# Kernel optimization log

Hardware: AMD Instinct MI355X
Metric: run time of the kernel (lower is better)

## Reference

```python
import jax, jax.numpy as jnp
import numpy as np
from itertools import combinations

# Module config: I=16, J=8 -> n_qubits = I + I + J = 40, k = 2
N_QUBITS = 40
K = 2
GATES = [(i, i + 1) for i in range(N_QUBITS - 1)]  # 39 RBS gates (ladder)
BATCH = 64


def _build_rbs_matrices():
    """Replicates RBS_Unitaries: for each gate (a,b) over the Hamming-weight-K
    basis of N_QUBITS qubits, build (A, B, C) with U(theta) = cos(theta)*A + sin(theta)*B + C.
    A: identity on states where exactly one of (a,b) is occupied (cos part).
    B: antisymmetric coupling swapping occupation of a<->b (sin part).
    C: identity on states where a,b have equal occupation (untouched part).
    """
    basis = list(combinations(range(N_QUBITS), K))
    idx = {s: i for i, s in enumerate(basis)}
    D = len(basis)  # binom(40, 2) = 780
    G = len(GATES)
    A = np.zeros((G, D, D), np.float32)
    B = np.zeros((G, D, D), np.float32)
    C = np.zeros((G, D, D), np.float32)
    for g, (a, b) in enumerate(GATES):
        for s in basis:
            i = idx[s]
            in_a, in_b = (a in s), (b in s)
            if in_a != in_b:
                A[g, i, i] = 1.0
                if in_a:  # pair |..1_a..0_b..> with |..0_a..1_b..>
                    t = tuple(sorted((set(s) - {a}) | {b}))
                    j = idx[t]
                    B[g, j, i] = 1.0
                    B[g, i, j] = -1.0
            else:
                C[g, i, i] = 1.0
    return A, B, C


def setup_inputs() -> dict:
    key = jax.random.key(0)
    k1, k2 = jax.random.split(key)
    A, B, C = _build_rbs_matrices()
    D = A.shape[-1]
    input_state = jax.random.normal(k1, (BATCH, D, D), dtype=jnp.float32)
    angles = jax.random.uniform(k2, (len(GATES),), dtype=jnp.float32)  # torch.rand(()) per gate
    return {
        "input_state": input_state,
        "angles": angles,
        "A": jnp.asarray(A),
        "B": jnp.asarray(B),
        "C": jnp.asarray(C),
    }


def reference(input_state, angles, A, B, C):
    """Sequentially applies each RBS gate: rho <- U rho U^T (real matrices)."""
    rho0 = input_state.astype(jnp.float32)

    def step(rho, gate):
        Ag, Bg, Cg, th = gate
        U = jnp.cos(th) * Ag + jnp.sin(th) * Bg + Cg  # [D, D]
        rho = jnp.einsum('ij,bjk->bik', U, rho)        # U @ rho
        rho = jnp.einsum('bik,lk->bil', rho, U)        # (U rho) @ U^T
        return rho, None

    out, _ = jax.lax.scan(step, rho0, (A, B, C, angles))
    return out
```

## Files before the change

### kernel.cpp

```cpp
#include <hip/hip_runtime.h>

#define D   780
#define NG  39
#define NP  38
#define KT  16

__device__ __forceinline__ int pair_idx(int p, int q) {
  return (p * (79 - p)) / 2 + (q - p - 1);
}

__device__ __forceinline__ void build_tables(uint* tbl, float2* cs,
                                             const float* __restrict__ ang,
                                             int tid, int nthr) {
  for (int t = tid; t < NG * NP; t += nthr) {
    const int g = t / NP, p = t - g * NP;
    const int cc = (p < g) ? p : p + 2;
    const int g1 = g + 1;
    const int a0 = (g  < cc) ? g  : cc,  a1 = (g  < cc) ? cc : g;
    const int b0 = (g1 < cc) ? g1 : cc,  b1 = (g1 < cc) ? cc : g1;
    const uint i4 = (uint)pair_idx(a0, a1) * 4u;
    const uint j4 = (uint)pair_idx(b0, b1) * 4u;
    tbl[t] = (i4 << 16) | j4;
  }
  if (tid < NG) {
    float s, c;
    sincosf(ang[tid], &s, &c);
    cs[tid] = make_float2(c, s);
  }
}

__device__ __forceinline__ void run_chain(float* __restrict__ v,
                                          const uint* __restrict__ tbl,
                                          const float2* __restrict__ cs,
                                          int lane) {
  char* vb = (char*)v;
  if (lane < NP) {
    #pragma unroll
    for (int g = 0; g < NG; ++g) {
      const uint pk = tbl[g * NP + lane];
      const float2 sc = cs[g];
      float* pi = (float*)(vb + (pk >> 16));
      float* pj = (float*)(vb + (pk & 0xffffu));
      const float vi = *pi, vj = *pj;
      *pi = sc.x * vi - sc.y * vj;
      *pj = sc.y * vi + sc.x * vj;
      __builtin_amdgcn_wave_barrier();
    }
  }
}

__global__ __launch_bounds__(512) void rbs_col_kernel(
    const float* __restrict__ rho, const float* __restrict__ ang,
    float* __restrict__ out) {
  __shared__ uint   tbl[NG * NP];
  __shared__ float2 cs[NG];
  __shared__ float  vbuf[8][D];
  build_tables(tbl, cs, ang, threadIdx.x, 512);
  __syncthreads();

  const int wave = threadIdx.x >> 6, lane = threadIdx.x & 63;
  const size_t row = (size_t)blockIdx.x * 8 + wave;
  const float4* src = (const float4*)(rho + row * (size_t)D);
  float* v = vbuf[wave];
  float4* v4 = (float4*)v;

  for (int e = lane; e < D / 4; e += 64) v4[e] = src[e];
  __builtin_amdgcn_wave_barrier();

  run_chain(v, tbl, cs, lane);

  float4* dst = (float4*)(out + row * (size_t)D);
  for (int e = lane; e < D / 4; e += 64) dst[e] = v4[e];
}

__global__ __launch_bounds__(1024) void rbs_row_kernel(
    float* __restrict__ data, const float* __restrict__ ang) {
  __shared__ uint   tbl[NG * NP];
  __shared__ float2 cs[NG];
  __shared__ float  vb[KT][D];
  build_tables(tbl, cs, ang, threadIdx.x, 1024);

  const int b  = blockIdx.y;
  const int k0 = blockIdx.x * KT;
  const int ncols = (D - k0 < KT) ? (D - k0) : KT;
  float* base = data + (size_t)b * D * D + k0;

  const int fc = (threadIdx.x & 3) * 4;
  const int r0 = threadIdx.x >> 2;
  if (fc < ncols) {
    for (int r = r0; r < D; r += 256) {
      float4 x = *(const float4*)(base + (size_t)r * D + fc);
      vb[fc + 0][r] = x.x; vb[fc + 1][r] = x.y;
      vb[fc + 2][r] = x.z; vb[fc + 3][r] = x.w;
    }
  }
  __syncthreads();

  const int w = threadIdx.x >> 6, lane = threadIdx.x & 63;
  if (w < ncols) run_chain(vb[w], tbl, cs, lane);
  __syncthreads();

  if (fc < ncols) {
    for (int r = r0; r < D; r += 256) {
      float4 x = make_float4(vb[fc + 0][r], vb[fc + 1][r],
                             vb[fc + 2][r], vb[fc + 3][r]);
      *(float4*)(base + (size_t)r * D + fc) = x;
    }
  }
}

extern "C" void kernel_launch(void* const* d_in, const int* in_sizes, int n_in,
                              void* d_out, int out_size, void* d_ws, size_t ws_size,
                              hipStream_t stream) {
  const float* rho = (const float*)d_in[0];
  const float* ang = (const float*)d_in[1];
  float* out = (float*)d_out;
  const int batch = in_sizes[0] / (D * D);

  const int nrows = batch * D;
  rbs_col_kernel<<<dim3(nrows / 8), 512, 0, stream>>>(rho, ang, out);

  rbs_row_kernel<<<dim3((D + KT - 1) / KT, batch), 1024, 0, stream>>>(out, ang);
}
```

Baseline: 508.5 us.

## Batch 16 vectors per wave with float4 interleaved rotation chain

Both passes now load a 16-vector tile into LDS, interleaved so the 16 vectors sit next to each other for each element index. Each lane then applies every Givens rotation to four vectors at once with float4 LDS accesses. This replaces the old one-vector-per-wave chain, where only 38 of 64 lanes did scalar work. The pair-index table moves to a compile-time constant array padded to 48 entries, and the sin/cos values are computed per lane and broadcast with readlane, which removes the per-block table build. The cost is single-wave blocks that each use about 51KB of LDS, so occupancy and latency hiding are low, and the row pass loads scalars with poor coalescing.

Result: slower. 845.2 us (+66.2%).

```diff
diff --git a/kernel.cpp b/kernel.cpp
--- a/kernel.cpp
+++ b/kernel.cpp
@@ -1,111 +1,124 @@
 #include <hip/hip_runtime.h>
 
-#define D   780
-#define NG  39
-#define NP  38
-#define KT  16
+#define D    780
+#define NG   39
+#define NP   38
+#define NPP  48
+#define KT   16
+#define ROWS 800
 
-__device__ __forceinline__ int pair_idx(int p, int q) {
-  return (p * (79 - p)) / 2 + (q - p - 1);
+struct Tbl { unsigned v[NG][NPP]; };
+
+constexpr int cpair(int p, int q) { return p * (79 - p) / 2 + (q - p - 1); }
+
+constexpr Tbl make_tbl() {
+  Tbl t{};
+  for (int g = 0; g < NG; ++g)
+    for (int p = 0; p < NPP; ++p) {
+      int i, j;
+      if (p < NP) {
+        const int cc = (p < g) ? p : p + 2;
+        const int g1 = g + 1;
+        const int a0 = (g  < cc) ? g  : cc,  a1 = (g  < cc) ? cc : g;
+        const int b0 = (g1 < cc) ? g1 : cc,  b1 = (g1 < cc) ? cc : g1;
+        i = cpair(a0, a1);
+        j = cpair(b0, b1);
+      } else {
+        i = D + (p - NP);
+        j = D + 10 + (p - NP);
+      }
+      t.v[g][p] = ((unsigned)(j * KT) << 16) | (unsigned)(i * KT);
+    }
+  return t;
 }
 
-__device__ __forceinline__ void build_tables(uint* tbl, float2* cs,
-                                             const float* __restrict__ ang,
-                                             int tid, int nthr) {
-  for (int t = tid; t < NG * NP; t += nthr) {
-    const int g = t / NP, p = t - g * NP;
-    const int cc = (p < g) ? p : p + 2;
-    const int g1 = g + 1;
-    const int a0 = (g  < cc) ? g  : cc,  a1 = (g  < cc) ? cc : g;
-    const int b0 = (g1 < cc) ? g1 : cc,  b1 = (g1 < cc) ? cc : g1;
-    const uint i4 = (uint)pair_idx(a0, a1) * 4u;
-    const uint j4 = (uint)pair_idx(b0, b1) * 4u;
-    tbl[t] = (i4 << 16) | j4;
-  }
-  if (tid < NG) {
-    float s, c;
-    sincosf(ang[tid], &s, &c);
-    cs[tid] = make_float2(c, s);
+__device__ __constant__ Tbl g_tbl = make_tbl();
+
+__device__ __forceinline__ void run_chain(float* __restrict__ t,
+                                          const float* __restrict__ ang,
+                                          int lane) {
+  float vc = 1.0f, vs = 0.0f;
+  if (lane < NG) sincosf(ang[lane], &vs, &vc);
+  const int pq = lane >> 2;
+  const int q4 = (lane & 3) * 4;
+
+  #pragma unroll 1
+  for (int g = 0; g < NG; ++g) {
+    const float c = __int_as_float(__builtin_amdgcn_readlane(__float_as_int(vc), g));
+    const float s = __int_as_float(__builtin_amdgcn_readlane(__float_as_int(vs), g));
+    const unsigned* tg = g_tbl.v[g];
+    #pragma unroll
+    for (int it = 0; it < 3; ++it) {
+      const unsigned pk = tg[it * 16 + pq];
+      const int fi = (int)(pk & 0xffffu) + q4;
+      const int fj = (int)(pk >> 16) + q4;
+      float4 vi = *(const float4*)(t + fi);
+      float4 vj = *(const float4*)(t + fj);
+      float4 ni, nj;
+      ni.x = c * vi.x - s * vj.x;  nj.x = s * vi.x + c * vj.x;
+      ni.y = c * vi.y - s * vj.y;  nj.y = s * vi.y + c * vj.y;
+      ni.z = c * vi.z - s * vj.z;  nj.z = s * vi.z + c * vj.z;
+      ni.w = c * vi.w - s * vj.w;  nj.w = s * vi.w + c * vj.w;
+      *(float4*)(t + fi) = ni;
+      *(float4*)(t + fj) = nj;
+    }
+    __builtin_amdgcn_wave_barrier();
   }
 }
 
-__device__ __forceinline__ void run_chain(float* __restrict__ v,
-                                          const uint* __restrict__ tbl,
-                                          const float2* __restrict__ cs,
-                                          int lane) {
-  char* vb = (char*)v;
-  if (lane < NP) {
-    #pragma unroll
-    for (int g = 0; g < NG; ++g) {
-      const uint pk = tbl[g * NP + lane];
-      const float2 sc = cs[g];
-      float* pi = (float*)(vb + (pk >> 16));
-      float* pj = (float*)(vb + (pk & 0xffffu));
-      const float vi = *pi, vj = *pj;
-      *pi = sc.x * vi - sc.y * vj;
-      *pj = sc.y * vi + sc.x * vj;
-      __builtin_amdgcn_wave_barrier();
+__global__ __launch_bounds__(64) void rbs_rows(const float* __restrict__ rho,
+                                               const float* __restrict__ ang,
+                                               float* __restrict__ out) {
+  __shared__ float tile[ROWS * KT];
+  const int l = threadIdx.x;
+  const size_t mat = (size_t)blockIdx.y * D * D;
+  const int r = l & 15, cg = l >> 4;
+  const int R = blockIdx.x * KT + r;
+
+  if (R < D) {
+    const float* row = rho + mat + (size_t)R * D;
+    #pragma unroll 4
+    for (int m = 0; m < 195; ++m) {
+      const int c = cg + 4 * m;
+      tile[c * KT + r] = row[c];
+    }
+  }
+  __syncthreads();
+  run_chain(tile, ang, l);
+  __syncthreads();
+  if (R < D) {
+    float* row = out + mat + (size_t)R * D;
+    #pragma unroll 4
+    for (int m = 0; m < 195; ++m) {
+      const int c = cg + 4 * m;
+      row[c] = tile[c * KT + r];
     }
   }
 }
 
-__global__ __launch_bounds__(512) void rbs_col_kernel(
-    const float* __restrict__ rho, const float* __restrict__ ang,
-    float* __restrict__ out) {
-  __shared__ uint   tbl[NG * NP];
-  __shared__ float2 cs[NG];
-  __shared__ float  vbuf[8][D];
-  build_tables(tbl, cs, ang, threadIdx.x, 512);
-  __syncthreads();
+__global__ __launch_bounds__(64) void rbs_cols(float* __restrict__ data,
+                                               const float* __restrict__ ang) {
+  __shared__ float tile[ROWS * KT];
+  const int l = threadIdx.x;
+  const int k0 = blockIdx.x * KT;
+  float* base = data + (size_t)blockIdx.y * D * D + k0;
+  const int kk = (l & 3) * 4, rl = l >> 2;
+  const bool colok = (k0 + kk + 3) < D;
 
-  const int wave = threadIdx.x >> 6, lane = threadIdx.x & 63;
-  const size_t row = (size_t)blockIdx.x * 8 + wave;
-  const float4* src = (const float4*)(rho + row * (size_t)D);
-  float* v = vbuf[wave];
-  float4* v4 = (float4*)v;
-
-  for (int e = lane; e < D / 4; e += 64) v4[e] = src[e];
-  __builtin_amdgcn_wave_barrier();
-
-  run_chain(v, tbl, cs, lane);
-
-  float4* dst = (float4*)(out + row * (size_t)D);
-  for (int e = lane; e < D / 4; e += 64) dst[e] = v4[e];
-}
-
-__global__ __launch_bounds__(1024) void rbs_row_kernel(
-    float* __restrict__ data, const float* __restrict__ ang) {
-  __shared__ uint   tbl[NG * NP];
-  __shared__ float2 cs[NG];
-  __shared__ float  vb[KT][D];
-  build_tables(tbl, cs, ang, threadIdx.x, 1024);
-
-  const int b  = blockIdx.y;
-  const int k0 = blockIdx.x * KT;
-  const int ncols = (D - k0 < KT) ? (D - k0) : KT;
-  float* base = data + (size_t)b * D * D + k0;
-
-  const int fc = (threadIdx.x & 3) * 4;
-  const int r0 = threadIdx.x >> 2;
-  if (fc < ncols) {
-    for (int r = r0; r < D; r += 256) {
-      float4 x = *(const float4*)(base + (size_t)r * D + fc);
-      vb[fc + 0][r] = x.x; vb[fc + 1][r] = x.y;
-      vb[fc + 2][r] = x.z; vb[fc + 3][r] = x.w;
-    }
+  for (int m = 0; m < 49; ++m) {
+    const int rr = rl + 16 * m;
+    if (rr < D && colok)
+      *(float4*)(tile + rr * KT + kk) =
+          *(const float4*)(base + (size_t)rr * D + kk);
   }
   __syncthreads();
-
-  const int w = threadIdx.x >> 6, lane = threadIdx.x & 63;
-  if (w < ncols) run_chain(vb[w], tbl, cs, lane);
+  run_chain(tile, ang, l);
   __syncthreads();
-
-  if (fc < ncols) {
-    for (int r = r0; r < D; r += 256) {
-      float4 x = make_float4(vb[fc + 0][r], vb[fc + 1][r],
-                             vb[fc + 2][r], vb[fc + 3][r]);
-      *(float4*)(base + (size_t)r * D + fc) = x;
-    }
+  for (int m = 0; m < 49; ++m) {
+    const int rr = rl + 16 * m;
+    if (rr < D && colok)
+      *(float4*)(base + (size_t)rr * D + kk) =
+          *(const float4*)(tile + rr * KT + kk);
   }
 }
 
@@ -116,9 +129,8 @@
   const float* ang = (const float*)d_in[1];
   float* out = (float*)d_out;
   const int batch = in_sizes[0] / (D * D);
+  const int ntiles = (D + KT - 1) / KT;
 
-  const int nrows = batch * D;
-  rbs_col_kernel<<<dim3(nrows / 8), 512, 0, stream>>>(rho, ang, out);
-
-  rbs_row_kernel<<<dim3((D + KT - 1) / KT, batch), 1024, 0, stream>>>(out, ang);
+  rbs_rows<<<dim3(ntiles, batch), 64, 0, stream>>>(rho, ang, out);
+  rbs_cols<<<dim3(ntiles, batch), 64, 0, stream>>>(out, ang);
 }
```
